# Kernel tuning notes

Measured on AMD Instinct MI355X. Metric: run time of the kernel, lower is better.

## Reference

```python
import jax, jax.numpy as jnp
import numpy as np

D_MODEL = 1024
NUM_HEADS = 16
D_FF = 4096
EPS = 1e-6


def _layernorm(x, alpha, beta):
    # custom LN: alpha * (x - mean) / (std + eps) + beta, std is UNBIASED (ddof=1)
    mu = jnp.mean(x, axis=-1, keepdims=True)
    var = jnp.sum((x - mu) ** 2, axis=-1, keepdims=True) / (x.shape[-1] - 1)
    return alpha * (x - mu) / (jnp.sqrt(var) + EPS) + beta


def setup_inputs() -> dict:
    key = jax.random.key(0)
    ks = jax.random.split(key, 8)
    B, S, D, F = 1, 4096, D_MODEL, D_FF
    s = 0.02
    inp = {
        "x": jax.random.normal(ks[0], (B, S, D), dtype=jnp.float32),
        "Wq": jax.random.normal(ks[1], (D, D), dtype=jnp.float32) * s,
        "bq": jnp.zeros((D,), jnp.float32),
        "Wk": jax.random.normal(ks[2], (D, D), dtype=jnp.float32) * s,
        "bk": jnp.zeros((D,), jnp.float32),
        "Wv": jax.random.normal(ks[3], (D, D), dtype=jnp.float32) * s,
        "bv": jnp.zeros((D,), jnp.float32),
        "Wo": jax.random.normal(ks[4], (D, D), dtype=jnp.float32) * s,
        "bo": jnp.zeros((D,), jnp.float32),
        "ln1_a": jnp.ones((1,), jnp.float32),
        "ln1_b": jnp.zeros((1,), jnp.float32),
        "W1": jax.random.normal(ks[5], (D, F), dtype=jnp.float32) * s,
        "b1": jnp.zeros((F,), jnp.float32),
        "W2": jax.random.normal(ks[6], (F, D), dtype=jnp.float32) * s,
        "b2": jnp.zeros((D,), jnp.float32),
        "ln2_a": jnp.ones((1,), jnp.float32),
        "ln2_b": jnp.zeros((1,), jnp.float32),
    }
    return inp


def reference(x, Wq, bq, Wk, bk, Wv, bv, Wo, bo, ln1_a, ln1_b,
              W1, b1, W2, b2, ln2_a, ln2_b):
    B, S, D = x.shape
    H = NUM_HEADS
    dk = D // H

    # --- residual 1: pre-LN self-attention ---
    h = _layernorm(x, ln1_a, ln1_b)
    Q = (h @ Wq + bq).reshape(B, S, H, dk)
    K = (h @ Wk + bk).reshape(B, S, H, dk)
    V = (h @ Wv + bv).reshape(B, S, H, dk)
    scores = jnp.einsum("bqhd,bkhd->bhqk", Q, K) / jnp.sqrt(jnp.float32(dk))
    attn = jax.nn.softmax(scores, axis=-1)  # [B,H,S,S] materialized as in source
    ctx = jnp.einsum("bhqk,bkhd->bqhd", attn, V).reshape(B, S, D)
    x = x + (ctx @ Wo + bo)  # dropout=0 -> identity

    # --- residual 2: pre-LN feed-forward ---
    h2 = _layernorm(x, ln2_a, ln2_b)
    ffn = jax.nn.relu(h2 @ W1 + b1) @ W2 + b2
    return x + ffn
```

## Files before the change

### kernel.cpp

```cpp
#include <hip/hip_runtime.h>
#include <hip/hip_bf16.h>

typedef __attribute__((ext_vector_type(8))) __bf16 bf16x8;
typedef __attribute__((ext_vector_type(4))) float f32x4;
typedef __attribute__((ext_vector_type(4))) short sh4;
typedef __attribute__((ext_vector_type(8))) short sh8;

#define MFMA(a, b, c) __builtin_amdgcn_mfma_f32_16x16x32_bf16(a, b, c, 0, 0, 0)

#if __has_builtin(__builtin_amdgcn_exp2f)
#define EXP2(x) __builtin_amdgcn_exp2f(x)
#else
#define EXP2(x) exp2f(x)
#endif

union P8 { struct { sh4 lo, hi; } p; sh8 v; };

__device__ __forceinline__ sh4 pk4(float a, float b, float c, float d) {
    __hip_bfloat162 lo = __float22bfloat162_rn(float2{a, b});
    __hip_bfloat162 hi = __float22bfloat162_rn(float2{c, d});
    union { struct { __hip_bfloat162 lo, hi; } p; sh4 s; } u;
    u.p.lo = lo; u.p.hi = hi;
    return u.s;
}

__device__ __forceinline__ float ldany(const void* p, size_t i, bool f32) {
    return f32 ? ((const float*)p)[i] : (float)(((const __bf16*)p)[i]);
}

__global__ void prep_k(const void* wq, float* flag,
                       const void* bq, const void* bk, const void* bv, const void* bo,
                       const void* b1, const void* b2,
                       const void* l1a, const void* l1b, const void* l2a, const void* l2b,
                       __bf16* dst) {
    __shared__ float red[256];
    __shared__ float fls;
    int tid = threadIdx.x;
    const __bf16* p = (const __bf16*)wq;
    float mx = 0.f;
    for (int i = tid; i < 1024; i += 256) {
        float v = (float)p[i];
        if (v != v) mx = 2.f;
        v = fabsf(v);
        if (v > mx) mx = v;
    }
    red[tid] = mx;
    __syncthreads();
    for (int s = 128; s > 0; s >>= 1) {
        if (tid < s) red[tid] = fmaxf(red[tid], red[tid + s]);
        __syncthreads();
    }
    if (tid == 0) { fls = (red[0] > 1.0f) ? 1.f : 0.f; *flag = fls; }
    __syncthreads();
    bool f32 = fls > 0.5f;
    const void* srcs[10] = {bq, bk, bv, bo, b1, b2, l1a, l1b, l2a, l2b};
    const int offs[10] = {1024, 2048, 3072, 4096, 5120, 9216, 10240, 10241, 10242, 10243};
    const int ns[10]   = {1024, 1024, 1024, 1024, 4096, 1024, 1, 1, 1, 1};
    for (int t = 0; t < 10; ++t)
        for (int j = tid; j < ns[t]; j += blockDim.x)
            dst[offs[t] + j] = (__bf16)ldany(srcs[t], j, f32);
}

__device__ __forceinline__ void tr_body(const void* in, __bf16* out, int R, int C, bool f32,
                                        int bx, int by, int x, int y) {
    __shared__ __bf16 t[32][33];
    for (int i = 0; i < 32; i += 8)
        t[y + i][x] = (__bf16)ldany(in, (size_t)(by + y + i) * C + bx + x, f32);
    __syncthreads();
    for (int i = 0; i < 32; i += 8)
        out[(size_t)(bx + y + i) * R + by + x] = t[x][y + i];
}

__global__ void transpose_cvt(const void* in, __bf16* out, int R, int C, const float* flag) {
    tr_body(in, out, R, C, *flag > 0.5f, blockIdx.x * 32, blockIdx.y * 32,
            threadIdx.x, threadIdx.y);
}

__global__ void transpose4_cvt(const void* i0, const void* i1, const void* i2, const void* i3,
                               __bf16* o0, __bf16* o1, __bf16* o2, __bf16* o3,
                               const float* flag) {
    const void* in = blockIdx.z == 0 ? i0 : blockIdx.z == 1 ? i1 : blockIdx.z == 2 ? i2 : i3;
    __bf16* out = blockIdx.z == 0 ? o0 : blockIdx.z == 1 ? o1 : blockIdx.z == 2 ? o2 : o3;
    tr_body(in, out, 1024, 1024, *flag > 0.5f, blockIdx.x * 32, blockIdx.y * 32,
            threadIdx.x, threadIdx.y);
}

__global__ __launch_bounds__(256) void layernorm_k(const void* x, int xmode, const float* flag,
                                                   __bf16* out,
                                                   const __bf16* alpha, const __bf16* beta) {
    int row = blockIdx.x * 4 + (threadIdx.x >> 6);
    int lane = threadIdx.x & 63;
    bool f32 = xmode && (*flag > 0.5f);
    float v[16];
    if (f32) {
        const float4* xr = (const float4*)((const float*)x + (size_t)row * 1024 + lane * 16);
#pragma unroll
        for (int q = 0; q < 4; ++q) {
            float4 r = xr[q];
            v[q * 4 + 0] = r.x; v[q * 4 + 1] = r.y; v[q * 4 + 2] = r.z; v[q * 4 + 3] = r.w;
        }
    } else {
        const __bf16* xr = (const __bf16*)x + (size_t)row * 1024 + lane * 16;
        bf16x8 h0 = *(const bf16x8*)xr;
        bf16x8 h1 = *(const bf16x8*)(xr + 8);
#pragma unroll
        for (int i = 0; i < 8; ++i) { v[i] = (float)h0[i]; v[8 + i] = (float)h1[i]; }
    }
    float s = 0.f, ss = 0.f;
#pragma unroll
    for (int i = 0; i < 16; ++i) { s += v[i]; ss += v[i] * v[i]; }
#pragma unroll
    for (int o = 1; o < 64; o <<= 1) { s += __shfl_xor(s, o); ss += __shfl_xor(ss, o); }
    float mu = s * (1.f / 1024.f);
    float var = (ss - 1024.f * mu * mu) * (1.f / 1023.f);
    float inv = 1.f / (sqrtf(var) + 1e-6f);
    float al = (float)alpha[0], be = (float)beta[0];
    bf16x8 o0, o1;
#pragma unroll
    for (int i = 0; i < 8; ++i) {
        o0[i] = (__bf16)((v[i] - mu) * inv * al + be);
        o1[i] = (__bf16)((v[8 + i] - mu) * inv * al + be);
    }
    __bf16* orow = out + (size_t)row * 1024;
    *(bf16x8*)(orow + lane * 16) = o0;
    *(bf16x8*)(orow + lane * 16 + 8) = o1;
}

__device__ __forceinline__ void swz_store(__bf16* buf, int hh, int ktt, int rr2, int cc2,
                                          float v) {
    size_t off = (((size_t)hh * 64 + ktt) << 12) + rr2 * 64 +
                 (((cc2 >> 3) ^ (rr2 & 7)) << 3) + (cc2 & 7);
    buf[off] = (__bf16)v;
}

__global__ __launch_bounds__(256) void gemm_bt(const __bf16* __restrict__ A, int lda,
                                               const __bf16* __restrict__ Bt, int ldb,
                                               const __bf16* __restrict__ bias_n,
                                               const __bf16* __restrict__ bias_m,
                                               const void* res, int res_mode,
                                               const float* flag,
                                               void* C, int out_pf,
                                               int M, int N, int K, int relu,
                                               __bf16* swzbuf, int swz) {
    __shared__ __bf16 As[2][128 * 32];
    __shared__ __bf16 Bs[2][128 * 32];
    const int tid = threadIdx.x;
    const int m0 = blockIdx.y * 128;
    const int n0 = blockIdx.x * 128;
    const int w = tid >> 6, lane = tid & 63;
    const int wr = (w >> 1) * 64, wc = (w & 1) * 64;
    const int lm = lane & 15, lg = lane >> 4;
    const bool f32 = *flag > 0.5f;
    const bool rf32 = (res_mode == 2) && f32;
    const bool of32 = out_pf && f32;

    auto stage = [&](int buf, int k0) {
#pragma unroll
        for (int i = 0; i < 2; ++i) {
            int c = i * 256 + tid;
            int row = c >> 2, kk = (c & 3) * 8;
            __builtin_amdgcn_global_load_lds(
                (const __attribute__((address_space(1))) void*)(A + (size_t)(m0 + row) * lda + k0 + kk),
                (__attribute__((address_space(3))) void*)(As[buf] + c * 8), 16, 0, 0);
            __builtin_amdgcn_global_load_lds(
                (const __attribute__((address_space(1))) void*)(Bt + (size_t)(n0 + row) * ldb + k0 + kk),
                (__attribute__((address_space(3))) void*)(Bs[buf] + c * 8), 16, 0, 0);
        }
    };

    f32x4 acc[4][4] = {};
    stage(0, 0);
    int cur = 0;
    for (int k0 = 0; k0 < K; k0 += 32) {
        if (k0 + 32 < K) {
            stage(cur ^ 1, k0 + 32);
            asm volatile("s_waitcnt vmcnt(4)" ::: "memory");
        } else {
            asm volatile("s_waitcnt vmcnt(0)" ::: "memory");
        }
        __builtin_amdgcn_s_barrier();
        bf16x8 a[4], b[4];
#pragma unroll
        for (int t = 0; t < 4; ++t)
            a[t] = *(const bf16x8*)(As[cur] + (wr + t * 16 + lm) * 32 + lg * 8);
#pragma unroll
        for (int t = 0; t < 4; ++t)
            b[t] = *(const bf16x8*)(Bs[cur] + (wc + t * 16 + lm) * 32 + lg * 8);
#pragma unroll
        for (int mt = 0; mt < 4; ++mt)
#pragma unroll
            for (int nt = 0; nt < 4; ++nt)
                acc[mt][nt] = MFMA(a[mt], b[nt], acc[mt][nt]);
        asm volatile("s_waitcnt lgkmcnt(0)" ::: "memory");
        __builtin_amdgcn_sched_barrier(0);
        __builtin_amdgcn_s_barrier();
        cur ^= 1;
    }
#pragma unroll
    for (int mt = 0; mt < 4; ++mt) {
#pragma unroll
        for (int nt = 0; nt < 4; ++nt) {
            int col = n0 + wc + nt * 16 + lm;
            float bn = bias_n ? (float)bias_n[col] : 0.f;
#pragma unroll
            for (int r = 0; r < 4; ++r) {
                int row = m0 + wr + mt * 16 + lg * 4 + r;
                float vv = acc[mt][nt][r] + bn;
                if (bias_m) vv += (float)bias_m[row];
                if (relu) vv = fmaxf(vv, 0.f);
                if (swz == 1 && col >= 1024) {
                    swz_store(swzbuf, (col - 1024) >> 6, row >> 6, row & 63, (col - 1024) & 63, vv);
                } else if (swz == 2) {
                    swz_store(swzbuf, row >> 6, col >> 6, row & 63, col & 63, vv);
                } else {
                    size_t idx = (size_t)row * N + col;
                    if (res_mode) vv += rf32 ? ((const float*)res)[idx]
                                             : (float)(((const __bf16*)res)[idx]);
                    if (of32) ((float*)C)[idx] = vv;
                    else ((__bf16*)C)[idx] = (__bf16)vv;
                }
            }
        }
    }
}

__global__ __launch_bounds__(256) void gemm_n64(const __bf16* __restrict__ A, int lda,
                                                const __bf16* __restrict__ Bt, int ldb,
                                                const __bf16* __restrict__ bias_n,
                                                const __bf16* __restrict__ bias_m,
                                                const void* res, int res_mode,
                                                const float* flag,
                                                void* C, int out_pf,
                                                int M, int N, int K, int relu,
                                                __bf16* swzbuf, int swz) {
    __shared__ __bf16 As[2][128 * 64];
    __shared__ __bf16 Bs[2][64 * 64];
    const int tid = threadIdx.x;
    const int m0 = blockIdx.y * 128;
    const int n0 = blockIdx.x * 64;
    const int w = tid >> 6, lane = tid & 63;
    const int wr = (w >> 1) * 64, wc = (w & 1) * 32;
    const int lm = lane & 15, lg = lane >> 4;
    const int sw = lm & 7;
    const bool f32 = *flag > 0.5f;
    const bool rf32 = (res_mode == 2) && f32;
    const bool of32 = out_pf && f32;

    auto stage = [&](int buf, int k0) {
#pragma unroll
        for (int i = 0; i < 4; ++i) {
            int c = i * 256 + tid;
            int row = c >> 3, ch = c & 7;
            __builtin_amdgcn_global_load_lds(
                (const __attribute__((address_space(1))) void*)(A + (size_t)(m0 + row) * lda + k0 + ((ch ^ (row & 7)) << 3)),
                (__attribute__((address_space(3))) void*)(As[buf] + c * 8), 16, 0, 0);
        }
#pragma unroll
        for (int i = 0; i < 2; ++i) {
            int c = i * 256 + tid;
            int row = c >> 3, ch = c & 7;
            __builtin_amdgcn_global_load_lds(
                (const __attribute__((address_space(1))) void*)(Bt + (size_t)(n0 + row) * ldb + k0 + ((ch ^ (row & 7)) << 3)),
                (__attribute__((address_space(3))) void*)(Bs[buf] + c * 8), 16, 0, 0);
        }
    };

    f32x4 acc[4][2] = {};
    stage(0, 0);
    int cur = 0;
    for (int k0 = 0; k0 < K; k0 += 64) {
        if (k0 + 64 < K) {
            stage(cur ^ 1, k0 + 64);
            asm volatile("s_waitcnt vmcnt(6)" ::: "memory");
        } else {
            asm volatile("s_waitcnt vmcnt(0)" ::: "memory");
        }
        __builtin_amdgcn_s_barrier();
        bf16x8 a[4][2], b[2][2];
#pragma unroll
        for (int t = 0; t < 4; ++t)
#pragma unroll
            for (int h = 0; h < 2; ++h)
                a[t][h] = *(const bf16x8*)(As[cur] + (wr + t * 16 + lm) * 64 + ((((h << 2) | lg) ^ sw) << 3));
#pragma unroll
        for (int t = 0; t < 2; ++t)
#pragma unroll
            for (int h = 0; h < 2; ++h)
                b[t][h] = *(const bf16x8*)(Bs[cur] + (wc + t * 16 + lm) * 64 + ((((h << 2) | lg) ^ sw) << 3));
#pragma unroll
        for (int mt = 0; mt < 4; ++mt)
#pragma unroll
            for (int nt = 0; nt < 2; ++nt) {
                acc[mt][nt] = MFMA(a[mt][0], b[nt][0], acc[mt][nt]);
                acc[mt][nt] = MFMA(a[mt][1], b[nt][1], acc[mt][nt]);
            }
        asm volatile("s_waitcnt lgkmcnt(0)" ::: "memory");
        __builtin_amdgcn_sched_barrier(0);
        __builtin_amdgcn_s_barrier();
        cur ^= 1;
    }
#pragma unroll
    for (int mt = 0; mt < 4; ++mt) {
#pragma unroll
        for (int nt = 0; nt < 2; ++nt) {
            int col = n0 + wc + nt * 16 + lm;
            float bn = bias_n ? (float)bias_n[col] : 0.f;
#pragma unroll
            for (int r = 0; r < 4; ++r) {
                int row = m0 + wr + mt * 16 + lg * 4 + r;
                float vv = acc[mt][nt][r] + bn;
                if (bias_m) vv += (float)bias_m[row];
                if (relu) vv = fmaxf(vv, 0.f);
                if (swz == 2) {
                    swz_store(swzbuf, row >> 6, col >> 6, row & 63, col & 63, vv);
                } else {
                    size_t idx = (size_t)row * N + col;
                    if (res_mode) vv += rf32 ? ((const float*)res)[idx]
                                             : (float)(((const __bf16*)res)[idx]);
                    if (of32) ((float*)C)[idx] = vv;
                    else ((__bf16*)C)[idx] = (__bf16)vv;
                }
            }
        }
    }
}

__global__ __launch_bounds__(256) void attn_ks2(const __bf16* __restrict__ Q, int ldq,
                                                const __bf16* __restrict__ Kswz,
                                                const __bf16* __restrict__ Vswz,
                                                __bf16* __restrict__ Opart,
                                                float* __restrict__ lpart) {
    constexpr int S = 4096;
    __shared__ __bf16 lds[2 * 8192];
    const int h = blockIdx.y, z = blockIdx.z;
    const int q0 = blockIdx.x * 128;
    const int tid = threadIdx.x, w = tid >> 6, lane = tid & 63;
    const int lm = lane & 15, lg = lane >> 4;

    const __bf16* gK = Kswz + (((size_t)h * 64 + z * 32) << 12);
    const __bf16* gV = Vswz + (((size_t)h * 64 + z * 32) << 12);

    bf16x8 qf[2][2];
#pragma unroll
    for (int qc = 0; qc < 2; ++qc) {
        const __bf16* qp = Q + (size_t)(q0 + w * 32 + qc * 16 + lm) * ldq + h * 64;
        qf[qc][0] = *(const bf16x8*)(qp + lg * 8);
        qf[qc][1] = *(const bf16x8*)(qp + 32 + lg * 8);
#pragma unroll
        for (int hh = 0; hh < 2; ++hh) {
            bf16x8 t = qf[qc][hh];
#pragma unroll
            for (int i = 0; i < 8; ++i) t[i] = (__bf16)((float)t[i] * 0.1803368801f);
            qf[qc][hh] = t;
        }
    }
    bf16x8 ones8;
#pragma unroll
    for (int i = 0; i < 8; ++i) ones8[i] = (__bf16)1.f;

    f32x4 o_[4][2] = {};
    f32x4 l_[2] = {};

    auto issue = [&](int t) {
        __bf16* dK = lds + (t & 1) * 8192;
        __bf16* dV = dK + 4096;
        const __bf16* sK = gK + ((size_t)t << 12);
        const __bf16* sV = gV + ((size_t)t << 12);
#pragma unroll
        for (int i = 0; i < 2; ++i) {
            int c = i * 256 + tid;
            __builtin_amdgcn_global_load_lds(
                (const __attribute__((address_space(1))) void*)(sK + c * 8),
                (__attribute__((address_space(3))) void*)(dK + c * 8), 16, 0, 0);
            __builtin_amdgcn_global_load_lds(
                (const __attribute__((address_space(1))) void*)(sV + c * 8),
                (__attribute__((address_space(3))) void*)(dV + c * 8), 16, 0, 0);
        }
    };
    issue(0);
    for (int t = 0; t < 32; ++t) {
        __syncthreads();
        if (t < 31) issue(t + 1);
        const __bf16* Kt = lds + (t & 1) * 8192;
        const __bf16* Vt = Kt + 4096;

        P8 pb[2][2];
#pragma unroll
        for (int mt = 0; mt < 4; ++mt) {
            int rr = mt * 16 + lm;
            const __bf16* kr = Kt + rr * 64;
            bf16x8 kf0 = *(const bf16x8*)(kr + ((lg ^ (rr & 7)) << 3));
            bf16x8 kf1 = *(const bf16x8*)(kr + (((4 + lg) ^ (rr & 7)) << 3));
#pragma unroll
            for (int qc = 0; qc < 2; ++qc) {
                f32x4 s = (f32x4){0.f, 0.f, 0.f, 0.f};
                s = MFMA(kf0, qf[qc][0], s);
                s = MFMA(kf1, qf[qc][1], s);
                sh4 e = pk4(EXP2(s[0]), EXP2(s[1]), EXP2(s[2]), EXP2(s[3]));
                if (mt & 1) pb[mt >> 1][qc].p.hi = e;
                else        pb[mt >> 1][qc].p.lo = e;
            }
        }
#pragma unroll
        for (int mtd = 0; mtd < 4; ++mtd) {
            int rr = mtd * 16 + lm;
            const __bf16* vr = Vt + rr * 64;
#pragma unroll
            for (int cp = 0; cp < 2; ++cp) {
                int cbase = cp * 4 + (lg >> 1);
                P8 va;
                va.p.lo = *(const sh4*)(vr + ((cbase ^ (rr & 7)) << 3) + (lg & 1) * 4);
                va.p.hi = *(const sh4*)(vr + (((cbase + 2) ^ (rr & 7)) << 3) + (lg & 1) * 4);
                bf16x8 vab = __builtin_bit_cast(bf16x8, va.v);
                o_[mtd][0] = MFMA(vab, __builtin_bit_cast(bf16x8, pb[cp][0].v), o_[mtd][0]);
                o_[mtd][1] = MFMA(vab, __builtin_bit_cast(bf16x8, pb[cp][1].v), o_[mtd][1]);
            }
        }
#pragma unroll
        for (int cp = 0; cp < 2; ++cp) {
            l_[0] = MFMA(ones8, __builtin_bit_cast(bf16x8, pb[cp][0].v), l_[0]);
            l_[1] = MFMA(ones8, __builtin_bit_cast(bf16x8, pb[cp][1].v), l_[1]);
        }
    }

    __syncthreads();
#pragma unroll
    for (int qc = 0; qc < 2; ++qc) {
#pragma unroll
        for (int mtd = 0; mtd < 4; ++mtd) {
            sh4 ov = pk4(o_[mtd][qc][0], o_[mtd][qc][1], o_[mtd][qc][2], o_[mtd][qc][3]);
            *(sh4*)(lds + (w * 32 + qc * 16 + lm) * 72 + mtd * 16 + lg * 4) = ov;
        }
        if (lg == 0)
            lpart[(size_t)(h * 2 + z) * S + q0 + w * 32 + qc * 16 + lm] = l_[qc][0];
    }
    __syncthreads();
    __bf16* Ob = Opart + (((size_t)(h * 2 + z) * S + q0) << 6);
    int row = tid >> 1, co = (tid & 1) * 32;
#pragma unroll
    for (int b = 0; b < 4; ++b)
        *(uint4*)(Ob + row * 64 + co + b * 8) = *(const uint4*)(lds + row * 72 + co + b * 8);
}

__global__ __launch_bounds__(256) void attn_comb(const __bf16* __restrict__ Opart,
                                                 const float* __restrict__ lpart,
                                                 __bf16* __restrict__ ctx) {
    constexpr int S = 4096;
#pragma unroll
    for (int it = 0; it < 4; ++it) {
        int task = blockIdx.x * 1024 + it * 256 + threadIdx.x;
        int q = task >> 7, c8 = task & 127, h = c8 >> 3, d8 = (c8 & 7) * 8;
        const __bf16* p0 = Opart + (((size_t)(h * 2 + 0) * S + q) << 6) + d8;
        const __bf16* p1 = Opart + (((size_t)(h * 2 + 1) * S + q) << 6) + d8;
        float inv = 1.f / (lpart[(size_t)(h * 2 + 0) * S + q] + lpart[(size_t)(h * 2 + 1) * S + q]);
        bf16x8 a = *(const bf16x8*)p0, b = *(const bf16x8*)p1, o;
#pragma unroll
        for (int i = 0; i < 8; ++i) o[i] = (__bf16)(((float)a[i] + (float)b[i]) * inv);
        *(bf16x8*)(ctx + (size_t)q * 1024 + c8 * 8) = o;
    }
}

__global__ __launch_bounds__(256) void attn_v3(const __bf16* __restrict__ Q, int ldq,
                                               const __bf16* __restrict__ Kg, int ldk,
                                               const __bf16* __restrict__ VT,
                                               __bf16* __restrict__ ctx) {
    constexpr int S = 4096, D = 1024, LDT = 72;
    __shared__ __bf16 lds[128 * LDT];
    __bf16* Kt = lds;
    __bf16* Vt = lds + 64 * LDT;
    const int h = blockIdx.y;
    const int q0 = blockIdx.x * 128;
    const int tid = threadIdx.x, w = tid >> 6, lane = tid & 63;
    const int lm = lane & 15, lg = lane >> 4;
    bf16x8 qf[2][2];
#pragma unroll
    for (int qc = 0; qc < 2; ++qc) {
        const __bf16* qp = Q + (size_t)(q0 + w * 32 + qc * 16 + lm) * ldq + h * 64;
        qf[qc][0] = *(const bf16x8*)(qp + lg * 8);
        qf[qc][1] = *(const bf16x8*)(qp + 32 + lg * 8);
#pragma unroll
        for (int hh = 0; hh < 2; ++hh) {
            bf16x8 t = qf[qc][hh];
#pragma unroll
            for (int i = 0; i < 8; ++i) t[i] = (__bf16)((float)t[i] * 0.1803368801f);
            qf[qc][hh] = t;
        }
    }
    bf16x8 ones8;
#pragma unroll
    for (int i = 0; i < 8; ++i) ones8[i] = (__bf16)1.f;
    f32x4 o_[4][2] = {};
    f32x4 l_[2] = {};
    for (int kt = 0; kt < S / 64; ++kt) {
        __syncthreads();
#pragma unroll
        for (int i = 0; i < 2; ++i) {
            int c = i * 256 + tid;
            int rr = c >> 3, cc = (c & 7) * 8;
            *(uint4*)(Kt + rr * LDT + cc) =
                *(const uint4*)(Kg + (size_t)(kt * 64 + rr) * ldk + h * 64 + cc);
            *(uint4*)(Vt + rr * LDT + cc) =
                *(const uint4*)(VT + (size_t)(h * 64 + rr) * S + kt * 64 + cc);
        }
        __syncthreads();
        P8 pb[2][2];
#pragma unroll
        for (int mt = 0; mt < 4; ++mt) {
            bf16x8 kf0 = *(const bf16x8*)(Kt + (mt * 16 + lm) * LDT + lg * 8);
            bf16x8 kf1 = *(const bf16x8*)(Kt + (mt * 16 + lm) * LDT + 32 + lg * 8);
#pragma unroll
            for (int qc = 0; qc < 2; ++qc) {
                f32x4 s = (f32x4){0.f, 0.f, 0.f, 0.f};
                s = MFMA(kf0, qf[qc][0], s);
                s = MFMA(kf1, qf[qc][1], s);
                sh4 e = pk4(EXP2(s[0]), EXP2(s[1]), EXP2(s[2]), EXP2(s[3]));
                if (mt & 1) pb[mt >> 1][qc].p.hi = e;
                else        pb[mt >> 1][qc].p.lo = e;
            }
        }
#pragma unroll
        for (int mtd = 0; mtd < 4; ++mtd) {
            const __bf16* vrow = Vt + (mtd * 16 + lm) * LDT;
#pragma unroll
            for (int cp = 0; cp < 2; ++cp) {
                P8 va;
                va.p.lo = *(const sh4*)(vrow + cp * 32 + lg * 4);
                va.p.hi = *(const sh4*)(vrow + cp * 32 + 16 + lg * 4);
                bf16x8 vab = __builtin_bit_cast(bf16x8, va.v);
                o_[mtd][0] = MFMA(vab, __builtin_bit_cast(bf16x8, pb[cp][0].v), o_[mtd][0]);
                o_[mtd][1] = MFMA(vab, __builtin_bit_cast(bf16x8, pb[cp][1].v), o_[mtd][1]);
            }
        }
#pragma unroll
        for (int cp = 0; cp < 2; ++cp) {
            l_[0] = MFMA(ones8, __builtin_bit_cast(bf16x8, pb[cp][0].v), l_[0]);
            l_[1] = MFMA(ones8, __builtin_bit_cast(bf16x8, pb[cp][1].v), l_[1]);
        }
    }
    __syncthreads();
    float inv[2] = {1.f / l_[0][0], 1.f / l_[1][0]};
#pragma unroll
    for (int qc = 0; qc < 2; ++qc)
#pragma unroll
        for (int mtd = 0; mtd < 4; ++mtd)
#pragma unroll
            for (int r = 0; r < 4; ++r)
                lds[(w * 32 + qc * 16 + lm) * LDT + mtd * 16 + lg * 4 + r] =
                    (__bf16)(o_[mtd][qc][r] * inv[qc]);
    __syncthreads();
    int row = tid >> 1, cb = (tid & 1) * 32;
#pragma unroll
    for (int b = 0; b < 4; ++b)
        *(uint4*)(ctx + (size_t)(q0 + row) * D + h * 64 + cb + b * 8) =
            *(const uint4*)(lds + row * LDT + cb + b * 8);
}

extern "C" void kernel_launch(void* const* d_in, const int* in_sizes, int n_in,
                              void* d_out, int out_size, void* d_ws, size_t ws_size,
                              hipStream_t stream) {
    const void* x    = d_in[0];
    const void* Wq   = d_in[1];
    const void* bq   = d_in[2];
    const void* Wk   = d_in[3];
    const void* bk   = d_in[4];
    const void* Wv   = d_in[5];
    const void* bv   = d_in[6];
    const void* Wo   = d_in[7];
    const void* bo   = d_in[8];
    const void* ln1a = d_in[9];
    const void* ln1b = d_in[10];
    const void* W1   = d_in[11];
    const void* b1   = d_in[12];
    const void* W2   = d_in[13];
    const void* b2   = d_in[14];
    const void* ln2a = d_in[15];
    const void* ln2b = d_in[16];

    constexpr size_t M1 = 1u << 20;
    __bf16* ws = (__bf16*)d_ws;
    float* flagF = (float*)ws;
    __bf16* bmir = ws;
    dim3 tb(32, 8);
    const bool big = ws_size >= (size_t)(32.25 * 2 * M1) + 4096;

    prep_k<<<1, 256, 0, stream>>>(Wq, flagF, bq, bk, bv, bo, b1, b2,
                                  ln1a, ln1b, ln2a, ln2b, bmir);

    if (big) {
        __bf16* WqT = ws + M1 / 4;
        __bf16* WkT = WqT + M1;
        __bf16* WvT = ws + 2 * M1 + M1 / 4;
        __bf16* WoT = ws + 3 * M1 + M1 / 4;
        __bf16* W2T = ws + M1 / 4;
        float* lpart = (float*)(ws + M1 / 4);
        __bf16* hb  = ws + 4 * M1 + M1 / 4;
        __bf16* h2  = hb;
        __bf16* QKb = ws + 8 * M1 + M1 / 4;
        __bf16* x2  = QKb;
        __bf16* W1T = ws + 12 * M1 + M1 / 4;
        __bf16* Kswz = ws + 16 * M1 + M1 / 4;
        __bf16* ctx  = Kswz;
        __bf16* Vswz = ws + 20 * M1 + M1 / 4;
        __bf16* Opart = ws + 24 * M1 + M1 / 4;
        __bf16* f1  = ws + 16 * M1 + M1 / 4;

        transpose4_cvt<<<dim3(32, 32, 4), tb, 0, stream>>>(Wq, Wk, Wv, Wo,
                                                           WqT, WkT, WvT, WoT, flagF);
        layernorm_k<<<1024, 256, 0, stream>>>(x, 1, flagF, hb, bmir + 10240, bmir + 10241);
        gemm_bt<<<dim3(16, 32), 256, 0, stream>>>(hb, 1024, WqT, 1024, bmir + 1024, nullptr,
                                                  nullptr, 0, flagF, QKb, 0, 4096, 2048, 1024, 0,
                                                  Kswz, 1);
        gemm_n64<<<dim3(64, 8), 256, 0, stream>>>(WvT, 1024, hb, 1024, nullptr, bmir + 3072,
                                                  nullptr, 0, flagF, nullptr, 0, 1024, 4096, 1024, 0,
                                                  Vswz, 2);
        attn_ks2<<<dim3(32, 16, 2), 256, 0, stream>>>(QKb, 2048, Kswz, Vswz, Opart, lpart);
        attn_comb<<<512, 256, 0, stream>>>(Opart, lpart, ctx);
        transpose_cvt<<<dim3(128, 32), tb, 0, stream>>>(W1, W1T, 1024, 4096, flagF);
        gemm_n64<<<dim3(16, 32), 256, 0, stream>>>(ctx, 1024, WoT, 1024, bmir + 4096, nullptr,
                                                   x, 2, flagF, x2, 0, 4096, 1024, 1024, 0,
                                                   nullptr, 0);
        transpose_cvt<<<dim3(32, 128), tb, 0, stream>>>(W2, W2T, 4096, 1024, flagF);
        layernorm_k<<<1024, 256, 0, stream>>>(x2, 0, flagF, h2, bmir + 10242, bmir + 10243);
        gemm_bt<<<dim3(32, 32), 256, 0, stream>>>(h2, 1024, W1T, 1024, bmir + 5120, nullptr,
                                                  nullptr, 0, flagF, f1, 0, 4096, 4096, 1024, 1,
                                                  nullptr, 0);
        gemm_n64<<<dim3(16, 32), 256, 0, stream>>>(f1, 4096, W2T, 4096, bmir + 9216, nullptr,
                                                   x2, 1, flagF, d_out, 1, 4096, 1024, 4096, 0,
                                                   nullptr, 0);
    } else {
        constexpr size_t Qn = 1u << 18;
        __bf16* WqT = ws + Qn;
        __bf16* WoT = WqT;
        __bf16* WkT = ws + 5 * Qn;
        __bf16* WvT = ws + 9 * Qn;
        __bf16* hb  = ws + 13 * Qn;
        __bf16* f1q = hb;
        __bf16* ctx = ws + 29 * Qn;
        __bf16* W2T = ctx;
        __bf16* QKb = ws + 45 * Qn;
        __bf16* x2  = QKb;
        __bf16* Kb  = ws + 61 * Qn;
        __bf16* h2  = Kb;
        __bf16* VTb = ws + 77 * Qn;
        __bf16* W1T = VTb;
        transpose_cvt<<<dim3(32, 32), tb, 0, stream>>>(Wq, WqT, 1024, 1024, flagF);
        transpose_cvt<<<dim3(32, 32), tb, 0, stream>>>(Wk, WkT, 1024, 1024, flagF);
        transpose_cvt<<<dim3(32, 32), tb, 0, stream>>>(Wv, WvT, 1024, 1024, flagF);
        layernorm_k<<<1024, 256, 0, stream>>>(x, 1, flagF, hb, bmir + 10240, bmir + 10241);
        gemm_bt<<<dim3(8, 32), 256, 0, stream>>>(hb, 1024, WqT, 1024, bmir + 1024, nullptr,
                                                 nullptr, 0, flagF, QKb, 0, 4096, 1024, 1024, 0,
                                                 nullptr, 0);
        gemm_bt<<<dim3(8, 32), 256, 0, stream>>>(hb, 1024, WkT, 1024, bmir + 2048, nullptr,
                                                 nullptr, 0, flagF, Kb, 0, 4096, 1024, 1024, 0,
                                                 nullptr, 0);
        gemm_n64<<<dim3(64, 8), 256, 0, stream>>>(WvT, 1024, hb, 1024, nullptr, bmir + 3072,
                                                  nullptr, 0, flagF, VTb, 0, 1024, 4096, 1024, 0,
                                                  nullptr, 0);
        attn_v3<<<dim3(32, 16), 256, 0, stream>>>(QKb, 1024, Kb, 1024, VTb, ctx);
        transpose_cvt<<<dim3(32, 32), tb, 0, stream>>>(Wo, WoT, 1024, 1024, flagF);
        gemm_n64<<<dim3(16, 32), 256, 0, stream>>>(ctx, 1024, WoT, 1024, bmir + 4096, nullptr,
                                                   x, 2, flagF, x2, 0, 4096, 1024, 1024, 0,
                                                   nullptr, 0);
        layernorm_k<<<1024, 256, 0, stream>>>(x2, 0, flagF, h2, bmir + 10242, bmir + 10243);
        transpose_cvt<<<dim3(128, 32), tb, 0, stream>>>(W1, W1T, 1024, 4096, flagF);
        transpose_cvt<<<dim3(32, 128), tb, 0, stream>>>(W2, W2T, 4096, 1024, flagF);
        for (int ck = 0; ck < 2; ++ck) {
            gemm_bt<<<dim3(16, 32), 256, 0, stream>>>(h2, 1024, W1T + (size_t)ck * 2048 * 1024,
                                                      1024, bmir + 5120 + ck * 2048, nullptr,
                                                      nullptr, 0, flagF, f1q, 0, 4096, 2048, 1024, 1,
                                                      nullptr, 0);
            gemm_n64<<<dim3(16, 32), 256, 0, stream>>>(f1q, 2048, W2T + ck * 2048, 4096,
                                                       ck == 0 ? bmir + 9216 : nullptr, nullptr,
                                                       x2, 1, flagF, ck == 1 ? d_out : (void*)x2,
                                                       ck == 1 ? 1 : 0, 4096, 1024, 2048, 0,
                                                       nullptr, 0);
        }
    }
}
```

Baseline: 479.9 us.

## Fuse V projection into QKV GEMM and triple-buffer GEMM shared-memory pipeline

Both GEMM kernels move from double- to triple-buffered LDS staging, prefetching two K-tiles ahead with adjusted vmcnt waits to hide global load latency. The separate V-projection GEMM launch is removed. Instead, the Q/K GEMM is widened to N=3072, writes Q densely with stride 1024, and stores K and V directly into their swizzled attention layouts. The extra LDS per block may reduce occupancy, and the V output is now computed in a different (transposed) tile orientation.

Measured after the change: 493.5 us. +2.9%, slower.

```diff
diff --git a/kernel.cpp b/kernel.cpp
--- a/kernel.cpp
+++ b/kernel.cpp
@@ -142,8 +142,8 @@
                                                void* C, int out_pf,
                                                int M, int N, int K, int relu,
                                                __bf16* swzbuf, int swz) {
-    __shared__ __bf16 As[2][128 * 32];
-    __shared__ __bf16 Bs[2][128 * 32];
+    __shared__ __bf16 As[3][128 * 32];
+    __shared__ __bf16 Bs[3][128 * 32];
     const int tid = threadIdx.x;
     const int m0 = blockIdx.y * 128;
     const int n0 = blockIdx.x * 128;
@@ -170,10 +170,14 @@
 
     f32x4 acc[4][4] = {};
     stage(0, 0);
-    int cur = 0;
-    for (int k0 = 0; k0 < K; k0 += 32) {
-        if (k0 + 32 < K) {
-            stage(cur ^ 1, k0 + 32);
+    if (K > 32) stage(1, 32);
+    int t = 0;
+    for (int k0 = 0; k0 < K; k0 += 32, ++t) {
+        int cur = t % 3;
+        if (k0 + 64 < K) {
+            stage((t + 2) % 3, k0 + 64);
+            asm volatile("s_waitcnt vmcnt(8)" ::: "memory");
+        } else if (k0 + 32 < K) {
             asm volatile("s_waitcnt vmcnt(4)" ::: "memory");
         } else {
             asm volatile("s_waitcnt vmcnt(0)" ::: "memory");
@@ -181,11 +185,11 @@
         __builtin_amdgcn_s_barrier();
         bf16x8 a[4], b[4];
 #pragma unroll
-        for (int t = 0; t < 4; ++t)
-            a[t] = *(const bf16x8*)(As[cur] + (wr + t * 16 + lm) * 32 + lg * 8);
-#pragma unroll
-        for (int t = 0; t < 4; ++t)
-            b[t] = *(const bf16x8*)(Bs[cur] + (wc + t * 16 + lm) * 32 + lg * 8);
+        for (int q = 0; q < 4; ++q)
+            a[q] = *(const bf16x8*)(As[cur] + (wr + q * 16 + lm) * 32 + lg * 8);
+#pragma unroll
+        for (int q = 0; q < 4; ++q)
+            b[q] = *(const bf16x8*)(Bs[cur] + (wc + q * 16 + lm) * 32 + lg * 8);
 #pragma unroll
         for (int mt = 0; mt < 4; ++mt)
 #pragma unroll
@@ -194,7 +198,6 @@
         asm volatile("s_waitcnt lgkmcnt(0)" ::: "memory");
         __builtin_amdgcn_sched_barrier(0);
         __builtin_amdgcn_s_barrier();
-        cur ^= 1;
     }
 #pragma unroll
     for (int mt = 0; mt < 4; ++mt) {
@@ -208,8 +211,15 @@
                 float vv = acc[mt][nt][r] + bn;
                 if (bias_m) vv += (float)bias_m[row];
                 if (relu) vv = fmaxf(vv, 0.f);
-                if (swz == 1 && col >= 1024) {
-                    swz_store(swzbuf, (col - 1024) >> 6, row >> 6, row & 63, (col - 1024) & 63, vv);
+                if (swz == 1) {
+                    if (col >= 2048) {
+                        int d = col - 2048;
+                        swz_store(swzbuf + (1u << 22), d >> 6, row >> 6, d & 63, row & 63, vv);
+                    } else if (col >= 1024) {
+                        swz_store(swzbuf, (col - 1024) >> 6, row >> 6, row & 63, (col - 1024) & 63, vv);
+                    } else {
+                        ((__bf16*)C)[(size_t)row * 1024 + col] = (__bf16)vv;
+                    }
                 } else if (swz == 2) {
                     swz_store(swzbuf, row >> 6, col >> 6, row & 63, col & 63, vv);
                 } else {
@@ -233,8 +243,8 @@
                                                 void* C, int out_pf,
                                                 int M, int N, int K, int relu,
                                                 __bf16* swzbuf, int swz) {
-    __shared__ __bf16 As[2][128 * 64];
-    __shared__ __bf16 Bs[2][64 * 64];
+    __shared__ __bf16 As[3][128 * 64];
+    __shared__ __bf16 Bs[3][64 * 64];
     const int tid = threadIdx.x;
     const int m0 = blockIdx.y * 128;
     const int n0 = blockIdx.x * 64;
@@ -267,10 +277,14 @@
 
     f32x4 acc[4][2] = {};
     stage(0, 0);
-    int cur = 0;
-    for (int k0 = 0; k0 < K; k0 += 64) {
-        if (k0 + 64 < K) {
-            stage(cur ^ 1, k0 + 64);
+    if (K > 64) stage(1, 64);
+    int t = 0;
+    for (int k0 = 0; k0 < K; k0 += 64, ++t) {
+        int cur = t % 3;
+        if (k0 + 128 < K) {
+            stage((t + 2) % 3, k0 + 128);
+            asm volatile("s_waitcnt vmcnt(12)" ::: "memory");
+        } else if (k0 + 64 < K) {
             asm volatile("s_waitcnt vmcnt(6)" ::: "memory");
         } else {
             asm volatile("s_waitcnt vmcnt(0)" ::: "memory");
@@ -278,15 +292,15 @@
         __builtin_amdgcn_s_barrier();
         bf16x8 a[4][2], b[2][2];
 #pragma unroll
-        for (int t = 0; t < 4; ++t)
+        for (int q = 0; q < 4; ++q)
 #pragma unroll
             for (int h = 0; h < 2; ++h)
-                a[t][h] = *(const bf16x8*)(As[cur] + (wr + t * 16 + lm) * 64 + ((((h << 2) | lg) ^ sw) << 3));
-#pragma unroll
-        for (int t = 0; t < 2; ++t)
+                a[q][h] = *(const bf16x8*)(As[cur] + (wr + q * 16 + lm) * 64 + ((((h << 2) | lg) ^ sw) << 3));
+#pragma unroll
+        for (int q = 0; q < 2; ++q)
 #pragma unroll
             for (int h = 0; h < 2; ++h)
-                b[t][h] = *(const bf16x8*)(Bs[cur] + (wc + t * 16 + lm) * 64 + ((((h << 2) | lg) ^ sw) << 3));
+                b[q][h] = *(const bf16x8*)(Bs[cur] + (wc + q * 16 + lm) * 64 + ((((h << 2) | lg) ^ sw) << 3));
 #pragma unroll
         for (int mt = 0; mt < 4; ++mt)
 #pragma unroll
@@ -297,7 +311,6 @@
         asm volatile("s_waitcnt lgkmcnt(0)" ::: "memory");
         __builtin_amdgcn_sched_barrier(0);
         __builtin_amdgcn_s_barrier();
-        cur ^= 1;
     }
 #pragma unroll
     for (int mt = 0; mt < 4; ++mt) {
@@ -607,13 +620,10 @@
         transpose4_cvt<<<dim3(32, 32, 4), tb, 0, stream>>>(Wq, Wk, Wv, Wo,
                                                            WqT, WkT, WvT, WoT, flagF);
         layernorm_k<<<1024, 256, 0, stream>>>(x, 1, flagF, hb, bmir + 10240, bmir + 10241);
-        gemm_bt<<<dim3(16, 32), 256, 0, stream>>>(hb, 1024, WqT, 1024, bmir + 1024, nullptr,
-                                                  nullptr, 0, flagF, QKb, 0, 4096, 2048, 1024, 0,
+        gemm_bt<<<dim3(24, 32), 256, 0, stream>>>(hb, 1024, WqT, 1024, bmir + 1024, nullptr,
+                                                  nullptr, 0, flagF, QKb, 0, 4096, 3072, 1024, 0,
                                                   Kswz, 1);
-        gemm_n64<<<dim3(64, 8), 256, 0, stream>>>(WvT, 1024, hb, 1024, nullptr, bmir + 3072,
-                                                  nullptr, 0, flagF, nullptr, 0, 1024, 4096, 1024, 0,
-                                                  Vswz, 2);
-        attn_ks2<<<dim3(32, 16, 2), 256, 0, stream>>>(QKb, 2048, Kswz, Vswz, Opart, lpart);
+        attn_ks2<<<dim3(32, 16, 2), 256, 0, stream>>>(QKb, 1024, Kswz, Vswz, Opart, lpart);
         attn_comb<<<512, 256, 0, stream>>>(Opart, lpart, ctx);
         transpose_cvt<<<dim3(128, 32), tb, 0, stream>>>(W1, W1T, 1024, 4096, flagF);
         gemm_n64<<<dim3(16, 32), 256, 0, stream>>>(ctx, 1024, WoT, 1024, bmir + 4096, nullptr,
```
